# Kernel tuning notes

Hardware: AMD Instinct MI355X
Metric: run time of the kernel (lower is better)

Reference implementation:

```python
import jax, jax.numpy as jnp
import numpy as np
import math

NUM_HEADS = 16
ROPE_BASE = 10000.0


def apply_rope(t):
    # t: [B, H, S, D] with D even. Interleaved-pair rotary embedding (torchtune-style).
    D = t.shape[-1]
    S = t.shape[-2]
    inv_freq = 1.0 / (ROPE_BASE ** (jnp.arange(0, D, 2, dtype=jnp.float32) / D))  # [D/2]
    angles = jnp.arange(S, dtype=jnp.float32)[:, None] * inv_freq[None, :]  # [S, D/2]
    cos = jnp.cos(angles).astype(t.dtype)  # [S, D/2]
    sin = jnp.sin(angles).astype(t.dtype)
    t1 = t[..., 0::2]  # [B, H, S, D/2]
    t2 = t[..., 1::2]
    r1 = t1 * cos - t2 * sin
    r2 = t1 * sin + t2 * cos
    # interleave back
    out = jnp.stack([r1, r2], axis=-1).reshape(t.shape)
    return out


def setup_inputs() -> dict:
    key = jax.random.key(0)
    ks = jax.random.split(key, 6)
    B, S, D = 4, 2048, 2048
    s_in = 1.0 / math.sqrt(D)
    x = jax.random.normal(ks[0], (B, S, D), dtype=jnp.float32)
    wq = jax.random.normal(ks[1], (D, D), dtype=jnp.float32) * s_in
    wk = jax.random.normal(ks[2], (D, D), dtype=jnp.float32) * s_in
    wv = jax.random.normal(ks[3], (D, D), dtype=jnp.float32) * s_in
    wo = jax.random.normal(ks[4], (D, D), dtype=jnp.float32) * s_in
    bo = jnp.zeros((D,), dtype=jnp.float32)
    return {"x": x, "wq": wq, "wk": wk, "wv": wv, "wo": wo, "bo": bo}


def reference(x, wq, wk, wv, wo, bo):
    B, S, D = x.shape
    H = NUM_HEADS
    hd = D // H
    # QKV projections (nn.Linear: y = x @ W^T)
    q = (x @ wq.T).reshape(B, S, H, hd).transpose(0, 2, 1, 3)  # [B,H,S,hd]
    k = (x @ wk.T).reshape(B, S, H, hd).transpose(0, 2, 1, 3)
    v = (x @ wv.T).reshape(B, S, H, hd).transpose(0, 2, 1, 3)
    q = apply_rope(q)
    k = apply_rope(k)
    # causal SDPA (dropout_p = 0 in eval)
    scale = 1.0 / math.sqrt(hd)
    scores = jnp.einsum('bhqd,bhkd->bhqk', q, k) * scale  # [B,H,S,S]
    causal = jnp.tril(jnp.ones((S, S), dtype=bool))
    scores = jnp.where(causal, scores, jnp.finfo(scores.dtype).min)
    attn = jax.nn.softmax(scores, axis=-1)
    ctx = jnp.einsum('bhqk,bhkd->bqhd', attn, v).reshape(B, S, D)
    return ctx @ wo.T + bo
```

## Files before the change

### kernel.cpp

```cpp
#include <hip/hip_runtime.h>

typedef short short8 __attribute__((ext_vector_type(8)));
typedef float f32x4 __attribute__((ext_vector_type(4)));
typedef unsigned int u32x4 __attribute__((ext_vector_type(4)));
typedef unsigned short u16x4 __attribute__((ext_vector_type(4)));
typedef unsigned short u16x8 __attribute__((ext_vector_type(8)));

__device__ __forceinline__ unsigned short f2bf(float f) {
  unsigned int u = __builtin_bit_cast(unsigned int, f);
  u += 0x7fffu + ((u >> 16) & 1u);
  return (unsigned short)(u >> 16);
}
__device__ __forceinline__ float bf2f(unsigned short h) {
  unsigned int u = ((unsigned int)h) << 16;
  return __builtin_bit_cast(float, u);
}

__device__ __forceinline__ void gl16(const unsigned short* g, unsigned short* l) {
  __builtin_amdgcn_global_load_lds((const __attribute__((address_space(1))) unsigned int*)g,
                                   (__attribute__((address_space(3))) unsigned int*)l, 16, 0, 0);
}

#define BB 4
#define SS 2048
#define DD 2048
#define HH 16
#define HD 128
#define MM (BB * SS)

__global__ void cast_all(const float* __restrict__ x, const float* __restrict__ wq,
                         const float* __restrict__ wk, const float* __restrict__ wv,
                         const float* __restrict__ wo, unsigned short* __restrict__ xb,
                         unsigned short* __restrict__ wqb, unsigned short* __restrict__ wkb,
                         unsigned short* __restrict__ wvb, unsigned short* __restrict__ wob) {
  int i = blockIdx.x * blockDim.x + threadIdx.x;
  const int X4 = (MM * DD) / 4;
  const int W4 = (DD * DD) / 4;
  const float* src;
  unsigned short* dst;
  int off;
  if (i < X4) {
    src = x; dst = xb; off = i;
  } else {
    int t = i - X4;
    int w = t >> 20;
    off = t & (W4 - 1);
    src = (w == 0) ? wq : (w == 1) ? wk : (w == 2) ? wv : wo;
    dst = (w == 0) ? wqb : (w == 1) ? wkb : (w == 2) ? wvb : wob;
  }
  f32x4 v = ((const f32x4*)src)[off];
  u16x4 o;
  o[0] = f2bf(v[0]); o[1] = f2bf(v[1]); o[2] = f2bf(v[2]); o[3] = f2bf(v[3]);
  ((u16x4*)dst)[off] = o;
}

#define STGH(P, R0, t, h, moff)                                                     \
  do {                                                                              \
    const unsigned short* _s =                                                      \
        (P) + (size_t)((R0) + (h) * 128 + srow) * DD + (size_t)((t) * 64 + scol);   \
    gl16(_s, lds + (moff) + (h) * 8192 + wvi * 512);                                \
    gl16(_s + (size_t)64 * DD, lds + (moff) + (h) * 8192 + 4096 + wvi * 512);       \
  } while (0)

#define BARRIER asm volatile("s_barrier" ::: "memory")

__device__ __forceinline__ void gemm_core(const unsigned short* __restrict__ Ap,
                                          const unsigned short* __restrict__ Bp,
                                          unsigned short* lds, int rt, int ct,
                                          f32x4 (&acc)[8][4]) {
  const int tid = threadIdx.x;
  const int lane = tid & 63, wvi = tid >> 6;
  const int wm = wvi >> 2, wn = wvi & 3;
  const int quad = lane >> 4, l16 = lane & 15;
  const int srow = wvi * 8 + (lane >> 3);
  const int scol = ((lane & 7) ^ (lane >> 3)) << 3;
  const int ck0 = (quad ^ (l16 & 7)) << 3;
  const int ck1 = ((4 + quad) ^ (l16 & 7)) << 3;
  const int aro = (wm * 128 + l16) << 6;
  const int bro = (wn * 64 + l16) << 6;
  const int rb = rt * 256, cb = ct * 256;

#pragma unroll
  for (int i = 0; i < 8; ++i)
#pragma unroll
    for (int j = 0; j < 4; ++j) acc[i][j] = f32x4{0.f, 0.f, 0.f, 0.f};

  STGH(Bp, cb, 0, 0, 16384);
  STGH(Bp, cb, 0, 1, 16384);
  STGH(Ap, rb, 0, 0, 0);
  STGH(Ap, rb, 0, 1, 0);
  STGH(Bp, cb, 1, 0, 49152);
  STGH(Bp, cb, 1, 1, 49152);
  asm volatile("s_waitcnt vmcnt(4)" ::: "memory");
  BARRIER;

#pragma unroll 2
  for (int t = 0; t < 32; ++t) {
    const unsigned short* ab = lds + ((t & 1) << 15);
    const unsigned short* bb = ab + 16384;
    const int pn = ((t + 1) & 1) << 15;
    const int pc = ((t & 1) << 15) + 16384;
    short8 aq[4][2], b0f[2][2], b1f[2][2];

#pragma unroll
    for (int mi = 0; mi < 4; ++mi) {
      aq[mi][0] = __builtin_bit_cast(short8, *(const u32x4*)(ab + aro + mi * 1024 + ck0));
      aq[mi][1] = __builtin_bit_cast(short8, *(const u32x4*)(ab + aro + mi * 1024 + ck1));
    }
#pragma unroll
    for (int ni = 0; ni < 2; ++ni) {
      b0f[ni][0] = __builtin_bit_cast(short8, *(const u32x4*)(bb + bro + ni * 1024 + ck0));
      b0f[ni][1] = __builtin_bit_cast(short8, *(const u32x4*)(bb + bro + ni * 1024 + ck1));
    }
    if (t < 31) STGH(Ap, rb, t + 1, 0, pn);
    BARRIER;
    __builtin_amdgcn_s_setprio(1);
#pragma unroll
    for (int k = 0; k < 2; ++k)
#pragma unroll
      for (int mi = 0; mi < 4; ++mi)
#pragma unroll
        for (int ni = 0; ni < 2; ++ni)
          acc[mi][ni] =
              __builtin_amdgcn_mfma_f32_16x16x32_bf16(aq[mi][k], b0f[ni][k], acc[mi][ni], 0, 0, 0);
    __builtin_amdgcn_s_setprio(0);
    BARRIER;

#pragma unroll
    for (int ni = 0; ni < 2; ++ni) {
      b1f[ni][0] = __builtin_bit_cast(short8, *(const u32x4*)(bb + bro + 2048 + ni * 1024 + ck0));
      b1f[ni][1] = __builtin_bit_cast(short8, *(const u32x4*)(bb + bro + 2048 + ni * 1024 + ck1));
    }
    if (t < 31) STGH(Ap, rb, t + 1, 1, pn);
    BARRIER;
    __builtin_amdgcn_s_setprio(1);
#pragma unroll
    for (int k = 0; k < 2; ++k)
#pragma unroll
      for (int mi = 0; mi < 4; ++mi)
#pragma unroll
        for (int ni = 0; ni < 2; ++ni)
          acc[mi][2 + ni] = __builtin_amdgcn_mfma_f32_16x16x32_bf16(aq[mi][k], b1f[ni][k],
                                                                    acc[mi][2 + ni], 0, 0, 0);
    __builtin_amdgcn_s_setprio(0);
    BARRIER;

#pragma unroll
    for (int mi = 0; mi < 4; ++mi) {
      aq[mi][0] = __builtin_bit_cast(short8, *(const u32x4*)(ab + aro + 4096 + mi * 1024 + ck0));
      aq[mi][1] = __builtin_bit_cast(short8, *(const u32x4*)(ab + aro + 4096 + mi * 1024 + ck1));
    }
    if (t < 30) STGH(Bp, cb, t + 2, 0, pc);
    BARRIER;
    __builtin_amdgcn_s_setprio(1);
#pragma unroll
    for (int k = 0; k < 2; ++k)
#pragma unroll
      for (int mi = 0; mi < 4; ++mi)
#pragma unroll
        for (int ni = 0; ni < 2; ++ni)
          acc[4 + mi][2 + ni] = __builtin_amdgcn_mfma_f32_16x16x32_bf16(
              aq[mi][k], b1f[ni][k], acc[4 + mi][2 + ni], 0, 0, 0);
    __builtin_amdgcn_s_setprio(0);
    BARRIER;

    if (t < 30) STGH(Bp, cb, t + 2, 1, pc);
    BARRIER;
    __builtin_amdgcn_s_setprio(1);
#pragma unroll
    for (int k = 0; k < 2; ++k)
#pragma unroll
      for (int mi = 0; mi < 4; ++mi)
#pragma unroll
        for (int ni = 0; ni < 2; ++ni)
          acc[4 + mi][ni] = __builtin_amdgcn_mfma_f32_16x16x32_bf16(aq[mi][k], b0f[ni][k],
                                                                    acc[4 + mi][ni], 0, 0, 0);
    __builtin_amdgcn_s_setprio(0);
    if (t < 30) {
      asm volatile("s_waitcnt vmcnt(4)" ::: "memory");
      BARRIER;
    } else if (t == 30) {
      asm volatile("s_waitcnt vmcnt(0)" ::: "memory");
      BARRIER;
    }
  }
}

__global__ __launch_bounds__(512, 2) void gemm_qkv(const unsigned short* __restrict__ A,
                                                   const unsigned short* __restrict__ W0,
                                                   const unsigned short* __restrict__ W1,
                                                   const unsigned short* __restrict__ W2,
                                                   unsigned short* __restrict__ q_out,
                                                   unsigned short* __restrict__ k_out,
                                                   unsigned short* __restrict__ v_out) {
  __shared__ unsigned short lds[65536];
  const int id = (blockIdx.z << 8) | (blockIdx.y << 3) | blockIdx.x;
  const int nid = (id & 7) * 96 + (id >> 3);
  const int z = nid >> 8;
  const int rt = (nid & 255) >> 3, ct = nid & 7;
  const unsigned short* W = (z == 0) ? W0 : (z == 1) ? W1 : W2;
  unsigned short* outb = (z == 0) ? q_out : (z == 1) ? k_out : v_out;
  f32x4 acc[8][4];
  gemm_core(A, W, lds, rt, ct, acc);

  const int tid = threadIdx.x;
  const int lane = tid & 63, wvi = tid >> 6;
  const int wm = wvi >> 2, wn = wvi & 3;
  const int quad = lane >> 4, l16 = lane & 15;

  if (z == 2) {
#pragma unroll
    for (int mi = 0; mi < 8; ++mi)
#pragma unroll
      for (int ni = 0; ni < 4; ++ni)
#pragma unroll
        for (int r = 0; r < 4; ++r) {
          int row_g = rt * 256 + wm * 128 + mi * 16 + quad * 4 + r;
          int col_g = ct * 256 + wn * 64 + ni * 16 + l16;
          int b = row_g >> 11, s = row_g & (SS - 1);
          int h = col_g >> 7, d = col_g & (HD - 1);
          outb[(((size_t)(b * HH + h)) * SS + (size_t)s) * HD + (size_t)d] = f2bf(acc[mi][ni][r]);
        }
  } else {
    const float psc = (z == 0) ? 0.08838834764831845f : 1.0f;
    const bool odd = (l16 & 1) != 0;
    const float nl = -0.14391156831212936f;
    float inv4[4];
#pragma unroll
    for (int ni = 0; ni < 4; ++ni)
      inv4[ni] = __expf((float)((((wn * 64 + ni * 16 + l16) & 127) >> 1)) * nl);
#pragma unroll
    for (int mi = 0; mi < 8; ++mi)
#pragma unroll
      for (int ni = 0; ni < 4; ++ni)
#pragma unroll
        for (int r = 0; r < 4; ++r) {
          int row_g = rt * 256 + wm * 128 + mi * 16 + quad * 4 + r;
          int col_g = ct * 256 + wn * 64 + ni * 16 + l16;
          int b = row_g >> 11, s = row_g & (SS - 1);
          int h = col_g >> 7, d = col_g & (HD - 1);
          float v = acc[mi][ni][r];
          float p = __shfl_xor(v, 1, 64);
          float ang = (float)s * inv4[ni];
          float cs = __cosf(ang), sn = __sinf(ang);
          float o = (odd ? (p * sn + v * cs) : (v * cs - p * sn)) * psc;
          size_t rowbase = (((size_t)(b * HH + h)) * SS + (size_t)s) * HD;
          if (z == 1) {
            outb[rowbase + (size_t)((((d >> 3) ^ (s & 7)) << 3) | (d & 7))] = f2bf(o);
          } else {
            outb[rowbase + (size_t)d] = f2bf(o);
          }
        }
  }
}

__global__ __launch_bounds__(512, 2) void gemm_out(const unsigned short* __restrict__ A,
                                                   const unsigned short* __restrict__ W,
                                                   float* __restrict__ outf,
                                                   const float* __restrict__ bias) {
  __shared__ unsigned short lds[65536];
  const int id = (blockIdx.y << 3) | blockIdx.x;
  const int nid = (id & 7) * 32 + (id >> 3);
  const int rt = nid >> 3, ct = nid & 7;
  f32x4 acc[8][4];
  gemm_core(A, W, lds, rt, ct, acc);

  const int tid = threadIdx.x;
  const int lane = tid & 63, wvi = tid >> 6;
  const int wm = wvi >> 2, wn = wvi & 3;
  const int quad = lane >> 4, l16 = lane & 15;
#pragma unroll
  for (int mi = 0; mi < 8; ++mi)
#pragma unroll
    for (int ni = 0; ni < 4; ++ni)
#pragma unroll
      for (int r = 0; r < 4; ++r) {
        int row_g = rt * 256 + wm * 128 + mi * 16 + quad * 4 + r;
        int col_g = ct * 256 + wn * 64 + ni * 16 + l16;
        outf[(size_t)row_g * DD + col_g] = acc[mi][ni][r] + bias[col_g];
      }
}

__global__ __launch_bounds__(256, 2) void attn_kernel(const unsigned short* __restrict__ qb,
                                                      const unsigned short* __restrict__ kb,
                                                      const unsigned short* __restrict__ vb,
                                                      unsigned short* __restrict__ ctxb) {
  __shared__ unsigned short lds[32768];
  const int tid = threadIdx.x;
  const int g0 = blockIdx.x;
  const int g = (g0 & 7) * 128 + (g0 >> 3);
  const int bh = g >> 4;
  const int qa = 15 - (g & 15);
  const int lane = tid & 63, wvi = tid >> 6;
  const int quad = lane >> 4, l16 = lane & 15;
  const size_t bhq = (size_t)bh * SS * HD;
  const int qrow = qa * 128 + wvi * 32;
  const int b = bh >> 4, h = bh & (HH - 1);
  unsigned short* Pw = lds + 24576 + wvi * 2048;
  unsigned short* Vt = lds + 16384;
  const int kcol = l16 * 8;
  f32x4 zero = {0.f, 0.f, 0.f, 0.f};

  short8 qf[2][4];
#pragma unroll
  for (int rb = 0; rb < 2; ++rb)
#pragma unroll
    for (int ks = 0; ks < 4; ++ks)
      qf[rb][ks] = __builtin_bit_cast(
          short8,
          *(const u32x4*)(qb + bhq + (size_t)(qrow + rb * 16 + l16) * HD + ks * 32 + quad * 8));

  f32x4 acc[2][8];
#pragma unroll
  for (int rb = 0; rb < 2; ++rb)
#pragma unroll
    for (int dt = 0; dt < 8; ++dt) acc[rb][dt] = zero;
  float lpart[2][4] = {{0.f, 0.f, 0.f, 0.f}, {0.f, 0.f, 0.f, 0.f}};

  const int ntile = 2 * qa + 2;

  {
    u32x4 pva0, pvb0, pva1, pvb1;
    {
      const unsigned short* vs0 = vb + bhq + (size_t)(2 * (tid & 31)) * HD + (tid >> 5) * 8;
      pva0 = *(const u32x4*)vs0;
      pvb0 = *(const u32x4*)(vs0 + HD);
      const int u = tid + 256;
      const unsigned short* vs1 = vb + bhq + (size_t)(2 * (u & 31)) * HD + (u >> 5) * 8;
      pva1 = *(const u32x4*)vs1;
      pvb1 = *(const u32x4*)(vs1 + HD);
    }
#pragma unroll
    for (int r = 0; r < 4; ++r)
      gl16(kb + bhq + (size_t)(r * 16 + wvi * 4 + quad) * HD + kcol,
           lds + (r * 16 + wvi * 4) * 128);
    unsigned int* vw = (unsigned int*)Vt;
    {
      int rr = tid & 31, c = tid >> 5;
      u16x8 va = __builtin_bit_cast(u16x8, pva0);
      u16x8 vb2 = __builtin_bit_cast(u16x8, pvb0);
#pragma unroll
      for (int j = 0; j < 8; ++j)
        vw[(c * 8 + j) * 32 + (((rr >> 2) ^ j) << 2) + (rr & 3)] =
            (unsigned int)va[j] | ((unsigned int)vb2[j] << 16);
      const int u = tid + 256;
      rr = u & 31; c = u >> 5;
      va = __builtin_bit_cast(u16x8, pva1);
      vb2 = __builtin_bit_cast(u16x8, pvb1);
#pragma unroll
      for (int j = 0; j < 8; ++j)
        vw[(c * 8 + j) * 32 + (((rr >> 2) ^ j) << 2) + (rr & 3)] =
            (unsigned int)va[j] | ((unsigned int)vb2[j] << 16);
    }
    __syncthreads();
  }

  for (int kt = 0; kt < ntile; ++kt) {
    const int kv0 = kt * 64;
    const unsigned short* Kc = lds + (kt & 1) * 8192;
    const int nxt = ((kt + 1) & 1) * 8192;
    const bool hasnext = (kt + 1 < ntile);

    u32x4 pva0, pvb0, pva1, pvb1;
    if (hasnext) {
      const int kvn = kv0 + 64;
      const unsigned short* vs0 = vb + bhq + (size_t)(kvn + 2 * (tid & 31)) * HD + (tid >> 5) * 8;
      pva0 = *(const u32x4*)vs0;
      pvb0 = *(const u32x4*)(vs0 + HD);
      const int u = tid + 256;
      const unsigned short* vs1 = vb + bhq + (size_t)(kvn + 2 * (u & 31)) * HD + (u >> 5) * 8;
      pva1 = *(const u32x4*)vs1;
      pvb1 = *(const u32x4*)(vs1 + HD);
#pragma unroll
      for (int r = 0; r < 4; ++r)
        gl16(kb + bhq + (size_t)(kvn + r * 16 + wvi * 4 + quad) * HD + kcol,
             lds + nxt + (r * 16 + wvi * 4) * 128);
    }

    f32x4 sc0[4], sc1[4];
#pragma unroll
    for (int nt = 0; nt < 4; ++nt) {
      sc0[nt] = zero;
      sc1[nt] = zero;
#pragma unroll
      for (int ks = 0; ks < 4; ++ks) {
        short8 kf = __builtin_bit_cast(
            short8, *(const u32x4*)(Kc + (nt * 16 + l16) * 128 +
                                    (((ks * 4 + quad) ^ (l16 & 7)) << 3)));
        sc0[nt] = __builtin_amdgcn_mfma_f32_16x16x32_bf16(qf[0][ks], kf, sc0[nt], 0, 0, 0);
        sc1[nt] = __builtin_amdgcn_mfma_f32_16x16x32_bf16(qf[1][ks], kf, sc1[nt], 0, 0, 0);
      }
    }

    const bool dm = (kt >= ntile - 2);
    if (dm) {
#pragma unroll
      for (int r = 0; r < 4; ++r) {
        int p15 = quad * 4 + r;
#pragma unroll
        for (int nt = 0; nt < 4; ++nt) {
          int col = kv0 + nt * 16 + l16;
          int el = p15 * 64 + ((((nt * 2 + (l16 >> 3)) + p15 + 4 * (p15 >> 3)) & 7) << 3) +
                   (l16 & 7);
          float pv0 = (col > qrow + p15) ? 0.f : __expf(sc0[nt][r]);
          lpart[0][r] += pv0;
          Pw[el] = f2bf(pv0);
          float pv1 = (col > qrow + 16 + p15) ? 0.f : __expf(sc1[nt][r]);
          lpart[1][r] += pv1;
          Pw[1024 + el] = f2bf(pv1);
        }
      }
    } else {
#pragma unroll
      for (int r = 0; r < 4; ++r) {
        int p15 = quad * 4 + r;
#pragma unroll
        for (int nt = 0; nt < 4; ++nt) {
          int el = p15 * 64 + ((((nt * 2 + (l16 >> 3)) + p15 + 4 * (p15 >> 3)) & 7) << 3) +
                   (l16 & 7);
          float pv0 = __expf(sc0[nt][r]);
          lpart[0][r] += pv0;
          Pw[el] = f2bf(pv0);
          float pv1 = __expf(sc1[nt][r]);
          lpart[1][r] += pv1;
          Pw[1024 + el] = f2bf(pv1);
        }
      }
    }

#pragma unroll
    for (int ks2 = 0; ks2 < 2; ++ks2) {
      const int pk = (((ks2 * 4 + quad) + l16 + 4 * (l16 >> 3)) & 7) << 3;
      short8 pf0 = __builtin_bit_cast(short8, *(const u32x4*)(Pw + l16 * 64 + pk));
      short8 pf1 = __builtin_bit_cast(short8, *(const u32x4*)(Pw + 1024 + l16 * 64 + pk));
#pragma unroll
      for (int dt = 0; dt < 8; ++dt) {
        short8 vf = __builtin_bit_cast(
            short8, *(const u32x4*)(Vt + (dt * 16 + l16) * 64 +
                                    (((ks2 * 4 + quad) ^ (l16 & 7)) << 3)));
        acc[0][dt] = __builtin_amdgcn_mfma_f32_16x16x32_bf16(pf0, vf, acc[0][dt], 0, 0, 0);
        acc[1][dt] = __builtin_amdgcn_mfma_f32_16x16x32_bf16(pf1, vf, acc[1][dt], 0, 0, 0);
      }
    }

    __syncthreads();

    if (hasnext) {
      unsigned int* vw = (unsigned int*)Vt;
      int rr = tid & 31, c = tid >> 5;
      u16x8 va = __builtin_bit_cast(u16x8, pva0);
      u16x8 vb2 = __builtin_bit_cast(u16x8, pvb0);
#pragma unroll
      for (int j = 0; j < 8; ++j)
        vw[(c * 8 + j) * 32 + (((rr >> 2) ^ j) << 2) + (rr & 3)] =
            (unsigned int)va[j] | ((unsigned int)vb2[j] << 16);
      const int u = tid + 256;
      rr = u & 31; c = u >> 5;
      va = __builtin_bit_cast(u16x8, pva1);
      vb2 = __builtin_bit_cast(u16x8, pvb1);
#pragma unroll
      for (int j = 0; j < 8; ++j)
        vw[(c * 8 + j) * 32 + (((rr >> 2) ^ j) << 2) + (rr & 3)] =
            (unsigned int)va[j] | ((unsigned int)vb2[j] << 16);
      __syncthreads();
    }
  }

#pragma unroll
  for (int rb = 0; rb < 2; ++rb) {
    float rl[4];
#pragma unroll
    for (int r = 0; r < 4; ++r) {
      float rs = lpart[rb][r];
#pragma unroll
      for (int off = 1; off < 16; off <<= 1) rs += __shfl_xor(rs, off, 64);
      rl[r] = 1.0f / rs;
    }
#pragma unroll
    for (int dt = 0; dt < 8; ++dt)
#pragma unroll
      for (int r = 0; r < 4; ++r) {
        int row = qrow + rb * 16 + quad * 4 + r;
        ctxb[((size_t)(b * SS + row)) * DD + h * HD + dt * 16 + l16] =
            f2bf(acc[rb][dt][r] * rl[r]);
      }
  }
}

extern "C" void kernel_launch(void* const* d_in, const int* in_sizes, int n_in,
                              void* d_out, int out_size, void* d_ws, size_t ws_size,
                              hipStream_t stream) {
  const float* x = (const float*)d_in[0];
  const float* wq = (const float*)d_in[1];
  const float* wk = (const float*)d_in[2];
  const float* wv = (const float*)d_in[3];
  const float* wo = (const float*)d_in[4];
  const float* bo = (const float*)d_in[5];
  float* out = (float*)d_out;

  unsigned short* xb = (unsigned short*)d_ws;
  unsigned short* wqb = xb + (size_t)MM * DD;
  unsigned short* wkb = wqb + (size_t)DD * DD;
  unsigned short* wvb = wkb + (size_t)DD * DD;
  unsigned short* wob = wvb + (size_t)DD * DD;
  unsigned short* qb = wob + (size_t)DD * DD;
  unsigned short* kb = qb + (size_t)MM * DD;
  unsigned short* vb = kb + (size_t)MM * DD;
  unsigned short* ctxb = vb + (size_t)MM * DD;

  cast_all<<<(2 * MM * DD / 4) / 256, 256, 0, stream>>>(x, wq, wk, wv, wo, xb, wqb, wkb, wvb, wob);

  dim3 gg(DD / 256, MM / 256, 3);
  gemm_qkv<<<gg, 512, 0, stream>>>(xb, wqb, wkb, wvb, qb, kb, vb);

  attn_kernel<<<1024, 256, 0, stream>>>(qb, kb, vb, ctxb);

  dim3 go(DD / 256, MM / 256);
  gemm_out<<<go, 512, 0, stream>>>(ctxb, wob, out, bo);
}
```

Measured before the change: 542.0 us.

## Shrink GEMM tiles to 256x128 with 4 waves and K-step 32

```diff
diff --git a/kernel.cpp b/kernel.cpp
--- a/kernel.cpp
+++ b/kernel.cpp
@@ -54,15 +54,20 @@
   ((u16x4*)dst)[off] = o;
 }
 
-#define STGH(P, R0, t, h, moff)                                                     \
+#define BARRIER asm volatile("s_barrier" ::: "memory")
+
+#define STGA(P, R0, t, bufo)                                                        \
   do {                                                                              \
-    const unsigned short* _s =                                                      \
-        (P) + (size_t)((R0) + (h) * 128 + srow) * DD + (size_t)((t) * 64 + scol);   \
-    gl16(_s, lds + (moff) + (h) * 8192 + wvi * 512);                                \
-    gl16(_s + (size_t)64 * DD, lds + (moff) + (h) * 8192 + 4096 + wvi * 512);       \
+    _Pragma("unroll") for (int i_ = 0; i_ < 4; ++i_)                                \
+        gl16((P) + (size_t)((R0) + i_ * 64 + srow) * DD + (size_t)((t) * 32 + scol),\
+             lds + (bufo) + i_ * 2048 + wvi * 512);                                 \
   } while (0)
-
-#define BARRIER asm volatile("s_barrier" ::: "memory")
+#define STGB(P, C0, t, bufo)                                                        \
+  do {                                                                              \
+    _Pragma("unroll") for (int i_ = 0; i_ < 2; ++i_)                                \
+        gl16((P) + (size_t)((C0) + i_ * 64 + srow) * DD + (size_t)((t) * 32 + scol),\
+             lds + (bufo) + 8192 + i_ * 2048 + wvi * 512);                          \
+  } while (0)
 
 __device__ __forceinline__ void gemm_core(const unsigned short* __restrict__ Ap,
                                           const unsigned short* __restrict__ Bp,
@@ -70,134 +75,88 @@
                                           f32x4 (&acc)[8][4]) {
   const int tid = threadIdx.x;
   const int lane = tid & 63, wvi = tid >> 6;
-  const int wm = wvi >> 2, wn = wvi & 3;
+  const int wm = wvi >> 1, wn = wvi & 1;
   const int quad = lane >> 4, l16 = lane & 15;
-  const int srow = wvi * 8 + (lane >> 3);
-  const int scol = ((lane & 7) ^ (lane >> 3)) << 3;
-  const int ck0 = (quad ^ (l16 & 7)) << 3;
-  const int ck1 = ((4 + quad) ^ (l16 & 7)) << 3;
-  const int aro = (wm * 128 + l16) << 6;
-  const int bro = (wn * 64 + l16) << 6;
-  const int rb = rt * 256, cb = ct * 256;
+  const int sg = tid >> 3;
+  const int ch = (tid & 7) ^ (sg & 7);
+  const int srow = (sg << 1) | (ch >> 2);
+  const int scol = (ch & 3) << 3;
+  const int ckA = (((((l16 & 1) << 2) | quad) ^ ((l16 >> 1) & 7)) << 3);
+  const int arow = wm * 64 + (l16 >> 1);
+  const int brow = wn * 32 + (l16 >> 1);
+  const int rb = rt * 256, cb = ct * 128;
 
 #pragma unroll
   for (int i = 0; i < 8; ++i)
 #pragma unroll
     for (int j = 0; j < 4; ++j) acc[i][j] = f32x4{0.f, 0.f, 0.f, 0.f};
 
-  STGH(Bp, cb, 0, 0, 16384);
-  STGH(Bp, cb, 0, 1, 16384);
-  STGH(Ap, rb, 0, 0, 0);
-  STGH(Ap, rb, 0, 1, 0);
-  STGH(Bp, cb, 1, 0, 49152);
-  STGH(Bp, cb, 1, 1, 49152);
-  asm volatile("s_waitcnt vmcnt(4)" ::: "memory");
+  STGB(Bp, cb, 0, 0);
+  STGA(Ap, rb, 0, 0);
+  STGB(Bp, cb, 1, 12288);
+  asm volatile("s_waitcnt vmcnt(2)" ::: "memory");
   BARRIER;
 
 #pragma unroll 2
-  for (int t = 0; t < 32; ++t) {
-    const unsigned short* ab = lds + ((t & 1) << 15);
-    const unsigned short* bb = ab + 16384;
-    const int pn = ((t + 1) & 1) << 15;
-    const int pc = ((t & 1) << 15) + 16384;
-    short8 aq[4][2], b0f[2][2], b1f[2][2];
-
-#pragma unroll
-    for (int mi = 0; mi < 4; ++mi) {
-      aq[mi][0] = __builtin_bit_cast(short8, *(const u32x4*)(ab + aro + mi * 1024 + ck0));
-      aq[mi][1] = __builtin_bit_cast(short8, *(const u32x4*)(ab + aro + mi * 1024 + ck1));
-    }
-#pragma unroll
-    for (int ni = 0; ni < 2; ++ni) {
-      b0f[ni][0] = __builtin_bit_cast(short8, *(const u32x4*)(bb + bro + ni * 1024 + ck0));
-      b0f[ni][1] = __builtin_bit_cast(short8, *(const u32x4*)(bb + bro + ni * 1024 + ck1));
-    }
-    if (t < 31) STGH(Ap, rb, t + 1, 0, pn);
+  for (int t = 0; t < 64; ++t) {
+    const unsigned short* ab = lds + (t & 1) * 12288;
+    const unsigned short* bb = ab + 8192;
+    const int bufn = ((t + 1) & 1) * 12288;
+    const int bufc = (t & 1) * 12288;
+    short8 aq[4], bf[4];
+
+#pragma unroll
+    for (int mi = 0; mi < 4; ++mi)
+      aq[mi] = __builtin_bit_cast(short8, *(const u32x4*)(ab + (arow + mi * 8) * 64 + ckA));
+#pragma unroll
+    for (int ni = 0; ni < 4; ++ni)
+      bf[ni] = __builtin_bit_cast(short8, *(const u32x4*)(bb + (brow + ni * 8) * 64 + ckA));
+    if (t < 63) STGA(Ap, rb, t + 1, bufn);
     BARRIER;
     __builtin_amdgcn_s_setprio(1);
 #pragma unroll
-    for (int k = 0; k < 2; ++k)
-#pragma unroll
-      for (int mi = 0; mi < 4; ++mi)
-#pragma unroll
-        for (int ni = 0; ni < 2; ++ni)
-          acc[mi][ni] =
-              __builtin_amdgcn_mfma_f32_16x16x32_bf16(aq[mi][k], b0f[ni][k], acc[mi][ni], 0, 0, 0);
+    for (int mi = 0; mi < 4; ++mi)
+#pragma unroll
+      for (int ni = 0; ni < 4; ++ni)
+        acc[mi][ni] = __builtin_amdgcn_mfma_f32_16x16x32_bf16(aq[mi], bf[ni], acc[mi][ni], 0, 0, 0);
     __builtin_amdgcn_s_setprio(0);
     BARRIER;
 
 #pragma unroll
-    for (int ni = 0; ni < 2; ++ni) {
-      b1f[ni][0] = __builtin_bit_cast(short8, *(const u32x4*)(bb + bro + 2048 + ni * 1024 + ck0));
-      b1f[ni][1] = __builtin_bit_cast(short8, *(const u32x4*)(bb + bro + 2048 + ni * 1024 + ck1));
-    }
-    if (t < 31) STGH(Ap, rb, t + 1, 1, pn);
+    for (int mi = 0; mi < 4; ++mi)
+      aq[mi] = __builtin_bit_cast(short8, *(const u32x4*)(ab + (arow + 32 + mi * 8) * 64 + ckA));
+    if (t < 62) STGB(Bp, cb, t + 2, bufc);
     BARRIER;
     __builtin_amdgcn_s_setprio(1);
 #pragma unroll
-    for (int k = 0; k < 2; ++k)
-#pragma unroll
-      for (int mi = 0; mi < 4; ++mi)
-#pragma unroll
-        for (int ni = 0; ni < 2; ++ni)
-          acc[mi][2 + ni] = __builtin_amdgcn_mfma_f32_16x16x32_bf16(aq[mi][k], b1f[ni][k],
-                                                                    acc[mi][2 + ni], 0, 0, 0);
+    for (int mi = 0; mi < 4; ++mi)
+#pragma unroll
+      for (int ni = 0; ni < 4; ++ni)
+        acc[4 + mi][ni] =
+            __builtin_amdgcn_mfma_f32_16x16x32_bf16(aq[mi], bf[ni], acc[4 + mi][ni], 0, 0, 0);
     __builtin_amdgcn_s_setprio(0);
-    BARRIER;
-
-#pragma unroll
-    for (int mi = 0; mi < 4; ++mi) {
-      aq[mi][0] = __builtin_bit_cast(short8, *(const u32x4*)(ab + aro + 4096 + mi * 1024 + ck0));
-      aq[mi][1] = __builtin_bit_cast(short8, *(const u32x4*)(ab + aro + 4096 + mi * 1024 + ck1));
-    }
-    if (t < 30) STGH(Bp, cb, t + 2, 0, pc);
-    BARRIER;
-    __builtin_amdgcn_s_setprio(1);
-#pragma unroll
-    for (int k = 0; k < 2; ++k)
-#pragma unroll
-      for (int mi = 0; mi < 4; ++mi)
-#pragma unroll
-        for (int ni = 0; ni < 2; ++ni)
-          acc[4 + mi][2 + ni] = __builtin_amdgcn_mfma_f32_16x16x32_bf16(
-              aq[mi][k], b1f[ni][k], acc[4 + mi][2 + ni], 0, 0, 0);
-    __builtin_amdgcn_s_setprio(0);
-    BARRIER;
-
-    if (t < 30) STGH(Bp, cb, t + 2, 1, pc);
-    BARRIER;
-    __builtin_amdgcn_s_setprio(1);
-#pragma unroll
-    for (int k = 0; k < 2; ++k)
-#pragma unroll
-      for (int mi = 0; mi < 4; ++mi)
-#pragma unroll
-        for (int ni = 0; ni < 2; ++ni)
-          acc[4 + mi][ni] = __builtin_amdgcn_mfma_f32_16x16x32_bf16(aq[mi][k], b0f[ni][k],
-                                                                    acc[4 + mi][ni], 0, 0, 0);
-    __builtin_amdgcn_s_setprio(0);
-    if (t < 30) {
-      asm volatile("s_waitcnt vmcnt(4)" ::: "memory");
+    if (t < 62) {
+      asm volatile("s_waitcnt vmcnt(2)" ::: "memory");
       BARRIER;
-    } else if (t == 30) {
+    } else if (t == 62) {
       asm volatile("s_waitcnt vmcnt(0)" ::: "memory");
       BARRIER;
     }
   }
 }
 
-__global__ __launch_bounds__(512, 2) void gemm_qkv(const unsigned short* __restrict__ A,
+__global__ __launch_bounds__(256, 2) void gemm_qkv(const unsigned short* __restrict__ A,
                                                    const unsigned short* __restrict__ W0,
                                                    const unsigned short* __restrict__ W1,
                                                    const unsigned short* __restrict__ W2,
                                                    unsigned short* __restrict__ q_out,
                                                    unsigned short* __restrict__ k_out,
                                                    unsigned short* __restrict__ v_out) {
-  __shared__ unsigned short lds[65536];
-  const int id = (blockIdx.z << 8) | (blockIdx.y << 3) | blockIdx.x;
-  const int nid = (id & 7) * 96 + (id >> 3);
-  const int z = nid >> 8;
-  const int rt = (nid & 255) >> 3, ct = nid & 7;
+  __shared__ unsigned short lds[24576];
+  const int id = (blockIdx.z << 9) | (blockIdx.y << 4) | blockIdx.x;
+  const int nid = (id & 7) * 192 + (id >> 3);
+  const int z = nid >> 9;
+  const int rt = (nid >> 4) & 31, ct = nid & 15;
   const unsigned short* W = (z == 0) ? W0 : (z == 1) ? W1 : W2;
   unsigned short* outb = (z == 0) ? q_out : (z == 1) ? k_out : v_out;
   f32x4 acc[8][4];
@@ -205,7 +164,7 @@
 
   const int tid = threadIdx.x;
   const int lane = tid & 63, wvi = tid >> 6;
-  const int wm = wvi >> 2, wn = wvi & 3;
+  const int wm = wvi >> 1, wn = wvi & 1;
   const int quad = lane >> 4, l16 = lane & 15;
 
   if (z == 2) {
@@ -216,7 +175,7 @@
 #pragma unroll
         for (int r = 0; r < 4; ++r) {
           int row_g = rt * 256 + wm * 128 + mi * 16 + quad * 4 + r;
-          int col_g = ct * 256 + wn * 64 + ni * 16 + l16;
+          int col_g = ct * 128 + wn * 64 + ni * 16 + l16;
           int b = row_g >> 11, s = row_g & (SS - 1);
           int h = col_g >> 7, d = col_g & (HD - 1);
           outb[(((size_t)(b * HH + h)) * SS + (size_t)s) * HD + (size_t)d] = f2bf(acc[mi][ni][r]);
@@ -228,7 +187,7 @@
     float inv4[4];
 #pragma unroll
     for (int ni = 0; ni < 4; ++ni)
-      inv4[ni] = __expf((float)((((wn * 64 + ni * 16 + l16) & 127) >> 1)) * nl);
+      inv4[ni] = __expf((float)((wn * 64 + ni * 16 + l16) >> 1) * nl);
 #pragma unroll
     for (int mi = 0; mi < 8; ++mi)
 #pragma unroll
@@ -236,7 +195,7 @@
 #pragma unroll
         for (int r = 0; r < 4; ++r) {
           int row_g = rt * 256 + wm * 128 + mi * 16 + quad * 4 + r;
-          int col_g = ct * 256 + wn * 64 + ni * 16 + l16;
+          int col_g = ct * 128 + wn * 64 + ni * 16 + l16;
           int b = row_g >> 11, s = row_g & (SS - 1);
           int h = col_g >> 7, d = col_g & (HD - 1);
           float v = acc[mi][ni][r];
@@ -254,20 +213,20 @@
   }
 }
 
-__global__ __launch_bounds__(512, 2) void gemm_out(const unsigned short* __restrict__ A,
+__global__ __launch_bounds__(256, 2) void gemm_out(const unsigned short* __restrict__ A,
                                                    const unsigned short* __restrict__ W,
                                                    float* __restrict__ outf,
                                                    const float* __restrict__ bias) {
-  __shared__ unsigned short lds[65536];
-  const int id = (blockIdx.y << 3) | blockIdx.x;
-  const int nid = (id & 7) * 32 + (id >> 3);
-  const int rt = nid >> 3, ct = nid & 7;
+  __shared__ unsigned short lds[24576];
+  const int id = (blockIdx.y << 4) | blockIdx.x;
+  const int nid = (id & 7) * 64 + (id >> 3);
+  const int rt = nid >> 4, ct = nid & 15;
   f32x4 acc[8][4];
   gemm_core(A, W, lds, rt, ct, acc);
 
   const int tid = threadIdx.x;
   const int lane = tid & 63, wvi = tid >> 6;
-  const int wm = wvi >> 2, wn = wvi & 3;
+  const int wm = wvi >> 1, wn = wvi & 1;
   const int quad = lane >> 4, l16 = lane & 15;
 #pragma unroll
   for (int mi = 0; mi < 8; ++mi)
@@ -276,7 +235,7 @@
 #pragma unroll
       for (int r = 0; r < 4; ++r) {
         int row_g = rt * 256 + wm * 128 + mi * 16 + quad * 4 + r;
-        int col_g = ct * 256 + wn * 64 + ni * 16 + l16;
+        int col_g = ct * 128 + wn * 64 + ni * 16 + l16;
         outf[(size_t)row_g * DD + col_g] = acc[mi][ni][r] + bias[col_g];
       }
 }
@@ -510,11 +469,11 @@
 
   cast_all<<<(2 * MM * DD / 4) / 256, 256, 0, stream>>>(x, wq, wk, wv, wo, xb, wqb, wkb, wvb, wob);
 
-  dim3 gg(DD / 256, MM / 256, 3);
-  gemm_qkv<<<gg, 512, 0, stream>>>(xb, wqb, wkb, wvb, qb, kb, vb);
+  dim3 gg(DD / 128, MM / 256, 3);
+  gemm_qkv<<<gg, 256, 0, stream>>>(xb, wqb, wkb, wvb, qb, kb, vb);
 
   attn_kernel<<<1024, 256, 0, stream>>>(qb, kb, vb, ctxb);
 
-  dim3 go(DD / 256, MM / 256);
-  gemm_out<<<go, 512, 0, stream>>>(ctxb, wob, out, bo);
-}
+  dim3 go(DD / 128, MM / 256);
+  gemm_out<<<go, 256, 0, stream>>>(ctxb, wob, out, bo);
+}
```

New measurement: 581.8 us. 1.07x slower.
